# Kernel tuning notes

Measured on AMD Instinct MI355X. Metric: run time of the kernel, lower is better.

Reference implementation:

```python
import jax, jax.numpy as jnp
import numpy as np

K_HEADS = 8
D_HEAD = 64
D = K_HEADS * D_HEAD  # 512
B, TP, TQ, N = 8, 48, 48, 256


def setup_inputs() -> dict:
    key = jax.random.key(0)
    ks = jax.random.split(key, 13)
    s = 1.0 / np.sqrt(D)
    inp = {
        "X": jax.random.normal(ks[0], (B, TP, N, D), jnp.float32),
        "STE_P": jax.random.normal(ks[1], (B, TP, N, D), jnp.float32),
        "STE_Q": jax.random.normal(ks[2], (B, TQ, N, D), jnp.float32),
        "Wq": jax.random.uniform(ks[3], (D, D), jnp.float32, -s, s),
        "bq": jax.random.uniform(ks[4], (D,), jnp.float32, -s, s),
        "Wk": jax.random.uniform(ks[5], (D, D), jnp.float32, -s, s),
        "bk": jax.random.uniform(ks[6], (D,), jnp.float32, -s, s),
        "Wv": jax.random.uniform(ks[7], (D, D), jnp.float32, -s, s),
        "bv": jax.random.uniform(ks[8], (D,), jnp.float32, -s, s),
        "W1": jax.random.uniform(ks[9], (D, D), jnp.float32, -s, s),
        "b1": jax.random.uniform(ks[10], (D,), jnp.float32, -s, s),
        "W2": jax.random.uniform(ks[11], (D, D), jnp.float32, -s, s),
        "b2": jax.random.uniform(ks[12], (D,), jnp.float32, -s, s),
    }
    return inp


def reference(X, STE_P, STE_Q, Wq, bq, Wk, bk, Wv, bv, W1, b1, W2, b2):
    # ReLU-fused QKV projections
    q = jax.nn.relu(STE_Q @ Wq + bq)  # [B, Tq, N, D]
    k = jax.nn.relu(STE_P @ Wk + bk)  # [B, Tp, N, D]
    v = jax.nn.relu(X @ Wv + bv)      # [B, Tp, N, D]

    # split(last, d) + cat(dim 0) == introduce head axis h of size K
    b, tq, n, _ = q.shape
    tp = k.shape[1]
    q = q.reshape(b, tq, n, K_HEADS, D_HEAD)
    k = k.reshape(b, tp, n, K_HEADS, D_HEAD)
    v = v.reshape(b, tp, n, K_HEADS, D_HEAD)

    # attention over the TIME axis, per node and head: scores [b,h,n,tq,tp]
    scale = 1.0 / jnp.sqrt(jnp.asarray(D_HEAD, q.dtype))
    attn = jnp.einsum('bqnhd,bpnhd->bhnqp', q, k) * scale
    attn = jax.nn.softmax(attn, axis=-1)
    out = jnp.einsum('bhnqp,bpnhd->bqnhd', attn, v).reshape(b, tq, n, D)

    out = jax.nn.relu(out @ W1 + b1) @ W2 + b2
    return out
```

## Files before the change

kernel.cpp:

```cpp
#include <hip/hip_runtime.h>

typedef _Float16 f16;
typedef __fp16 hf2 __attribute__((ext_vector_type(2)));
typedef _Float16 f16x4 __attribute__((ext_vector_type(4)));
typedef _Float16 f16x8 __attribute__((ext_vector_type(8)));
typedef float f32x4 __attribute__((ext_vector_type(4)));

typedef const __attribute__((address_space(1))) unsigned int guint;
typedef __attribute__((address_space(3))) unsigned int luint;
__device__ __forceinline__ void gl_lds16(const void* g, void* l) {
    __builtin_amdgcn_global_load_lds((guint*)g, (luint*)l, 16, 0, 0);
}
template <int N>
__device__ __forceinline__ void vmwait() {
    if constexpr (N == 8)       asm volatile("s_waitcnt vmcnt(8)" ::: "memory");
    else if constexpr (N == 6)  asm volatile("s_waitcnt vmcnt(6)" ::: "memory");
    else if constexpr (N == 4)  asm volatile("s_waitcnt vmcnt(4)" ::: "memory");
    else                        asm volatile("s_waitcnt vmcnt(0)" ::: "memory");
}
__device__ __forceinline__ void barrier_raw() { __builtin_amdgcn_s_barrier(); __builtin_amdgcn_sched_barrier(0); }

__global__ __launch_bounds__(256) void wconv(const float* w0, const float* w1, const float* w2,
                                             const float* w3, const float* w4, f16* dst) {
    const float* src;
    switch (blockIdx.z) { case 0: src = w0; break; case 1: src = w1; break;
                          case 2: src = w2; break; case 3: src = w3; break; default: src = w4; }
    __shared__ float tile[32][33];
    int k0 = blockIdx.x * 32, n0 = blockIdx.y * 32;
    int t = threadIdx.x;
    int r = t >> 3, c4 = (t & 7) * 4;
    float4 v = *(const float4*)(src + (k0 + r) * 512 + n0 + c4);
    tile[r][c4 + 0] = v.x; tile[r][c4 + 1] = v.y; tile[r][c4 + 2] = v.z; tile[r][c4 + 3] = v.w;
    __syncthreads();
    f16x4 o;
    o[0] = (f16)tile[c4 + 0][r]; o[1] = (f16)tile[c4 + 1][r];
    o[2] = (f16)tile[c4 + 2][r]; o[3] = (f16)tile[c4 + 3][r];
    *(f16x4*)(dst + (size_t)blockIdx.z * 262144 + (n0 + r) * 512 + k0 + c4) = o;
}

__global__ __launch_bounds__(512, 1) void gemm_qkv(const float* __restrict__ A,
                                                   const f16* __restrict__ Bt,
                                                   const float* __restrict__ bias,
                                                   f16* __restrict__ Cp) {
    constexpr int ASZ = 32768;
    constexpr int BUFSZ = ASZ + 16384;
    __shared__ __align__(16) char smem[3 * BUFSZ];

    const int cpx = gridDim.x >> 3;
    const int orig = blockIdx.x;
    const int wgid = (orig & 7) * cpx + (orig >> 3);
    const int by = wgid & 1;
    const int bx = wgid >> 1;
    const int r0 = bx * 256, c0 = by * 256;

    const int t = threadIdx.x;
    const int j = t & 63, w = t >> 6;
    const int lr = j & 15, lq = j >> 4;
    const int wr = (w >> 2) * 128, wc = (w & 3) * 64;

    const float* aS = A + (size_t)(r0 + (t >> 3)) * 512 + ((t & 7) ^ ((t >> 3) & 7)) * 4;
    const f16* bS = Bt + (size_t)(c0 + (t >> 2)) * 512 + ((t & 3) ^ ((t >> 3) & 3)) * 8;
    const int dstT = t * 16;

    int aoffL[8], aoffH[8], boff[4];
#pragma unroll
    for (int m = 0; m < 8; m++) {
        int row = wr + m * 16 + lr;
        int s = row & 7;
        aoffL[m] = row * 128 + (((2 * lq) ^ s) << 4);
        aoffH[m] = row * 128 + (((2 * lq + 1) ^ s) << 4);
    }
#pragma unroll
    for (int nb = 0; nb < 4; nb++) {
        int row = wc + nb * 16 + lr;
        boff[nb] = ASZ + row * 64 + ((lq ^ ((row >> 1) & 3)) << 4);
    }

    f32x4 acc[8][4] = {};

    auto stageA = [&](int kt, int buf) {
        char* d = smem + buf * BUFSZ + dstT;
        const float* s = aS + kt * 32;
#pragma unroll
        for (int i = 0; i < 4; i++) gl_lds16(s + (size_t)i * 64 * 512, d + i * 8192);
    };
    auto stageB = [&](int kt, int buf) {
        char* d = smem + buf * BUFSZ + ASZ + dstT;
        const f16* s = bS + kt * 32;
        gl_lds16(s, d);
        gl_lds16(s + 65536, d + 8192);
    };

    auto loadA4 = [&](const char* sb, int m0, f16x8* afr) {
#pragma unroll
        for (int m = 0; m < 4; m++) {
            float4 x0 = *(const float4*)(sb + aoffL[m0 + m]);
            float4 x1 = *(const float4*)(sb + aoffH[m0 + m]);
            hf2 p0 = __builtin_amdgcn_cvt_pkrtz(x0.x, x0.y);
            hf2 p1 = __builtin_amdgcn_cvt_pkrtz(x0.z, x0.w);
            hf2 p2 = __builtin_amdgcn_cvt_pkrtz(x1.x, x1.y);
            hf2 p3 = __builtin_amdgcn_cvt_pkrtz(x1.z, x1.w);
            f16x8 h;
            h[0] = (f16)p0[0]; h[1] = (f16)p0[1]; h[2] = (f16)p1[0]; h[3] = (f16)p1[1];
            h[4] = (f16)p2[0]; h[5] = (f16)p2[1]; h[6] = (f16)p3[0]; h[7] = (f16)p3[1];
            afr[m] = h;
        }
    };

    stageA(0, 0); stageB(0, 0); stageA(1, 1); stageB(1, 1);

    int bufc = 0;
#pragma unroll 1
    for (int kt = 0; kt < 16; ++kt) {
        const char* sb = smem + bufc * BUFSZ;
        const int bufs = (bufc == 2) ? 0 : bufc + 1;
        const int bufs2 = (bufs == 2) ? 0 : bufs + 1;
        if (kt < 15) vmwait<6>(); else vmwait<0>();
        barrier_raw();
        if (kt < 14) stageA(kt + 2, bufs2);
        f16x8 bfr[4], afr[4];
#pragma unroll
        for (int nb = 0; nb < 4; nb++) bfr[nb] = *(const f16x8*)(sb + boff[nb]);
        loadA4(sb, 0, afr);
        __builtin_amdgcn_s_setprio(1);
#pragma unroll
        for (int m = 0; m < 4; m++)
#pragma unroll
            for (int nb = 0; nb < 4; nb++)
                acc[m][nb] = __builtin_amdgcn_mfma_f32_16x16x32_f16(afr[m], bfr[nb], acc[m][nb], 0, 0, 0);
        __builtin_amdgcn_s_setprio(0);
        barrier_raw();
        if (kt < 14) stageB(kt + 2, bufs2);
        f16x8 afr2[4];
        loadA4(sb, 4, afr2);
        __builtin_amdgcn_s_setprio(1);
#pragma unroll
        for (int m = 0; m < 4; m++)
#pragma unroll
            for (int nb = 0; nb < 4; nb++)
                acc[m + 4][nb] = __builtin_amdgcn_mfma_f32_16x16x32_f16(afr2[m], bfr[nb], acc[m + 4][nb], 0, 0, 0);
        __builtin_amdgcn_s_setprio(0);
        bufc = bufs;
    }

#pragma unroll
    for (int nb = 0; nb < 4; nb++) {
        int col = c0 + wc + nb * 16 + lr;
        float b = bias[col];
#pragma unroll
        for (int m = 0; m < 8; m++) {
#pragma unroll
            for (int r = 0; r < 4; r++) {
                float v = fmaxf(acc[m][nb][r] + b, 0.0f);
                size_t row = (size_t)(r0 + wr + m * 16 + lq * 4 + r);
                Cp[row * 512 + col] = (f16)v;
            }
        }
    }
}

template <bool RELU, bool O16>
__global__ __launch_bounds__(512, 2) void gemm_8ph(const f16* __restrict__ A,
                                                   const f16* __restrict__ Bt,
                                                   const float* __restrict__ bias,
                                                   void* __restrict__ Cp) {
    constexpr int BUFSZ = 32768;
    __shared__ __align__(16) char smem[4 * BUFSZ];

    const int cpx = gridDim.x >> 3;
    const int orig = blockIdx.x;
    const int wgid = (orig & 7) * cpx + (orig >> 3);
    const int by = wgid & 1;
    const int bx = wgid >> 1;
    const int r0 = bx * 256, c0 = by * 256;

    const int t = threadIdx.x;
    const int j = t & 63, w = t >> 6;
    const int lr = j & 15, lq = j >> 4;
    const int wr = (w >> 2) * 128, wc = (w & 3) * 64;

    const int srow = t >> 2;
    const int sblk = (t & 3) ^ ((t >> 3) & 3);
    const f16* aS = A  + (size_t)(r0 + srow) * 512 + sblk * 8;
    const f16* bS = Bt + (size_t)(c0 + srow) * 512 + sblk * 8;
    const int dstT = t * 16;

    int aoff[8], boff[4];
#pragma unroll
    for (int m = 0; m < 8; m++) {
        int row = wr + m * 16 + lr;
        aoff[m] = row * 64 + ((lq ^ ((row >> 1) & 3)) << 4);
    }
#pragma unroll
    for (int nb = 0; nb < 4; nb++) {
        int row = wc + nb * 16 + lr;
        boff[nb] = 16384 + row * 64 + ((lq ^ ((row >> 1) & 3)) << 4);
    }

    f32x4 acc[8][4] = {};

    auto stageA = [&](int kt) {
        char* d = smem + (kt & 3) * BUFSZ + dstT;
        const f16* s = aS + kt * 32;
        gl_lds16(s, d);
        gl_lds16(s + 65536, d + 8192);
    };
    auto stageB = [&](int kt) {
        char* d = smem + (kt & 3) * BUFSZ + 16384 + dstT;
        const f16* s = bS + kt * 32;
        gl_lds16(s, d);
        gl_lds16(s + 65536, d + 8192);
    };

    stageA(0); stageB(0); stageA(1); stageB(1); stageA(2); stageB(2);

#pragma unroll 1
    for (int kt = 0; kt < 16; ++kt) {
        const char* sb = smem + (kt & 3) * BUFSZ;
        if (kt <= 13)      vmwait<8>();
        else if (kt == 14) vmwait<4>();
        else               vmwait<0>();
        barrier_raw();
        if (kt < 13) stageA(kt + 3);
        f16x8 bfr[4], afr[4];
#pragma unroll
        for (int nb = 0; nb < 4; nb++) bfr[nb] = *(const f16x8*)(sb + boff[nb]);
#pragma unroll
        for (int m = 0; m < 4; m++) afr[m] = *(const f16x8*)(sb + aoff[m]);
        __builtin_amdgcn_s_setprio(1);
#pragma unroll
        for (int m = 0; m < 4; m++)
#pragma unroll
            for (int nb = 0; nb < 4; nb++)
                acc[m][nb] = __builtin_amdgcn_mfma_f32_16x16x32_f16(afr[m], bfr[nb], acc[m][nb], 0, 0, 0);
        __builtin_amdgcn_s_setprio(0);
        barrier_raw();
        if (kt < 13) stageB(kt + 3);
        f16x8 afr2[4];
#pragma unroll
        for (int m = 0; m < 4; m++) afr2[m] = *(const f16x8*)(sb + aoff[m + 4]);
        __builtin_amdgcn_s_setprio(1);
#pragma unroll
        for (int m = 0; m < 4; m++)
#pragma unroll
            for (int nb = 0; nb < 4; nb++)
                acc[m + 4][nb] = __builtin_amdgcn_mfma_f32_16x16x32_f16(afr2[m], bfr[nb], acc[m + 4][nb], 0, 0, 0);
        __builtin_amdgcn_s_setprio(0);
    }

#pragma unroll
    for (int nb = 0; nb < 4; nb++) {
        int col = c0 + wc + nb * 16 + lr;
        float b = bias[col];
#pragma unroll
        for (int m = 0; m < 8; m++) {
#pragma unroll
            for (int r = 0; r < 4; r++) {
                float v = acc[m][nb][r] + b;
                if (RELU) v = fmaxf(v, 0.0f);
                size_t row = (size_t)(r0 + wr + m * 16 + lq * 4 + r);
                if (O16) ((f16*)Cp)[row * 512 + col] = (f16)v;
                else     ((float*)Cp)[row * 512 + col] = v;
            }
        }
    }
}

__global__ __launch_bounds__(64) void attn_kernel(const f16* __restrict__ q,
                                                  const f16* __restrict__ k,
                                                  const f16* __restrict__ v,
                                                  f16* __restrict__ out) {
    const int h = blockIdx.x, n = blockIdx.y, b = blockIdx.z;
    __shared__ f16 sQ[48 * 72];
    __shared__ f16 sK[48 * 72];
    __shared__ f16 sP[48 * 72];
    __shared__ f16 sVt[64 * 72];
    const int l = threadIdx.x, lr = l & 15, lq = l >> 4;
    const size_t rowstride = 256 * 512;
    const size_t base = ((size_t)(b * 48) * 256 + n) * 512 + h * 64;

    const int pr = l >> 3, pc = (l & 7) * 8;
#pragma unroll
    for (int pass = 0; pass < 6; pass++) {
        int row = pass * 8 + pr;
        size_t g = base + (size_t)row * rowstride + pc;
        f16x8 qv = *(const f16x8*)(q + g);
        f16x8 kv = *(const f16x8*)(k + g);
        f16x8 vv = *(const f16x8*)(v + g);
        *(f16x8*)&sQ[row * 72 + pc] = qv;
        *(f16x8*)&sK[row * 72 + pc] = kv;
#pragma unroll
        for (int jj = 0; jj < 8; jj++) sVt[(pc + jj) * 72 + row] = vv[jj];
    }
    {
        f16x8 z = {};
        *(f16x8*)&sVt[l * 72 + 48] = z;
        *(f16x8*)&sVt[l * 72 + 56] = z;
        if (l < 48) { *(f16x8*)&sP[l * 72 + 48] = z; *(f16x8*)&sP[l * 72 + 56] = z; }
    }
    __syncthreads();

    f32x4 s[3][3] = {};
#pragma unroll
    for (int ks = 0; ks < 2; ks++) {
        f16x8 aq[3], bk[3];
#pragma unroll
        for (int m = 0; m < 3; m++)  aq[m] = *(const f16x8*)&sQ[(m * 16 + lr) * 72 + ks * 32 + lq * 8];
#pragma unroll
        for (int nb = 0; nb < 3; nb++) bk[nb] = *(const f16x8*)&sK[(nb * 16 + lr) * 72 + ks * 32 + lq * 8];
#pragma unroll
        for (int m = 0; m < 3; m++)
#pragma unroll
            for (int nb = 0; nb < 3; nb++)
                s[m][nb] = __builtin_amdgcn_mfma_f32_16x16x32_f16(aq[m], bk[nb], s[m][nb], 0, 0, 0);
    }

#pragma unroll
    for (int m = 0; m < 3; m++) {
#pragma unroll
        for (int r = 0; r < 4; r++) {
            float a0 = s[m][0][r] * 0.125f, a1 = s[m][1][r] * 0.125f, a2 = s[m][2][r] * 0.125f;
            float mx = fmaxf(a0, fmaxf(a1, a2));
#pragma unroll
            for (int d = 1; d < 16; d <<= 1) mx = fmaxf(mx, __shfl_xor(mx, d));
            float e0 = __expf(a0 - mx), e1 = __expf(a1 - mx), e2 = __expf(a2 - mx);
            float sm = e0 + e1 + e2;
#pragma unroll
            for (int d = 1; d < 16; d <<= 1) sm += __shfl_xor(sm, d);
            float inv = 1.0f / sm;
            int row = m * 16 + lq * 4 + r;
            sP[row * 72 + 0  + lr] = (f16)(e0 * inv);
            sP[row * 72 + 16 + lr] = (f16)(e1 * inv);
            sP[row * 72 + 32 + lr] = (f16)(e2 * inv);
        }
    }
    __syncthreads();

    f32x4 o[3][4] = {};
#pragma unroll
    for (int ks = 0; ks < 2; ks++) {
        f16x8 ap[3], bvv[4];
#pragma unroll
        for (int m = 0; m < 3; m++)  ap[m] = *(const f16x8*)&sP[(m * 16 + lr) * 72 + ks * 32 + lq * 8];
#pragma unroll
        for (int nb = 0; nb < 4; nb++) bvv[nb] = *(const f16x8*)&sVt[(nb * 16 + lr) * 72 + ks * 32 + lq * 8];
#pragma unroll
        for (int m = 0; m < 3; m++)
#pragma unroll
            for (int nb = 0; nb < 4; nb++)
                o[m][nb] = __builtin_amdgcn_mfma_f32_16x16x32_f16(ap[m], bvv[nb], o[m][nb], 0, 0, 0);
    }

#pragma unroll
    for (int m = 0; m < 3; m++)
#pragma unroll
        for (int nb = 0; nb < 4; nb++)
#pragma unroll
            for (int r = 0; r < 4; r++) {
                int row = m * 16 + lq * 4 + r;
                out[base + (size_t)row * rowstride + nb * 16 + lr] = (f16)o[m][nb][r];
            }
}

extern "C" void kernel_launch(void* const* d_in, const int* in_sizes, int n_in,
                              void* d_out, int out_size, void* d_ws, size_t ws_size,
                              hipStream_t stream) {
    const float* X    = (const float*)d_in[0];
    const float* STEP = (const float*)d_in[1];
    const float* STEQ = (const float*)d_in[2];
    const float* Wq   = (const float*)d_in[3];
    const float* bq   = (const float*)d_in[4];
    const float* Wk   = (const float*)d_in[5];
    const float* bk   = (const float*)d_in[6];
    const float* Wv   = (const float*)d_in[7];
    const float* bv   = (const float*)d_in[8];
    const float* W1   = (const float*)d_in[9];
    const float* b1   = (const float*)d_in[10];
    const float* W2   = (const float*)d_in[11];
    const float* b2   = (const float*)d_in[12];
    float* out = (float*)d_out;

    const size_t MROWS = 98304;
    f16* ws  = (f16*)d_ws;
    f16* Wqt = ws;
    f16* Wkt = ws + 262144;
    f16* Wvt = ws + 524288;
    f16* W1t = ws + 786432;
    f16* W2t = ws + 1048576;
    f16* qb  = ws + 1310720;
    f16* kb  = qb + MROWS * 512;
    f16* vb  = kb + MROWS * 512;
    f16* attn = qb;
    f16* hb   = kb;

    wconv<<<dim3(16, 16, 5), 256, 0, stream>>>(Wq, Wk, Wv, W1, W2, ws);

    gemm_qkv<<<768, 512, 0, stream>>>(STEQ, Wqt, bq, qb);
    gemm_qkv<<<768, 512, 0, stream>>>(STEP, Wkt, bk, kb);
    gemm_qkv<<<768, 512, 0, stream>>>(X,    Wvt, bv, vb);

    attn_kernel<<<dim3(8, 256, 8), 64, 0, stream>>>(qb, kb, vb, attn);

    gemm_8ph<true,  true ><<<768, 512, 0, stream>>>(attn, W1t, b1, hb);
    gemm_8ph<false, false><<<768, 512, 0, stream>>>(hb,   W2t, b2, out);
}
```

Measured before the change: 674.6 us.

## Pre-convert QKV inputs to fp16 and use full-width 128-row GEMM tiles

A new conv3 kernel converts STE_Q, STE_P and X from fp32 to fp16 into the q/k/v workspace buffers. The QKV projection GEMM is replaced by gemm_f512, which reads fp16 A and computes a 128x512 output tile per block, writing in place over its own input rows. This removes the per-tile fp32-to-fp16 conversion and the large fp32 A staging in LDS. Because each block now covers all 512 output columns, A is read once per GEMM instead of once per column half. The cost is an extra pass over the activations to write and re-read fp16 copies, plus one more kernel launch.

```diff
diff --git a/kernel.cpp b/kernel.cpp
--- a/kernel.cpp
+++ b/kernel.cpp
@@ -14,11 +14,22 @@
 template <int N>
 __device__ __forceinline__ void vmwait() {
     if constexpr (N == 8)       asm volatile("s_waitcnt vmcnt(8)" ::: "memory");
-    else if constexpr (N == 6)  asm volatile("s_waitcnt vmcnt(6)" ::: "memory");
+    else if constexpr (N == 5)  asm volatile("s_waitcnt vmcnt(5)" ::: "memory");
     else if constexpr (N == 4)  asm volatile("s_waitcnt vmcnt(4)" ::: "memory");
     else                        asm volatile("s_waitcnt vmcnt(0)" ::: "memory");
 }
 __device__ __forceinline__ void barrier_raw() { __builtin_amdgcn_s_barrier(); __builtin_amdgcn_sched_barrier(0); }
+
+__device__ __forceinline__ f16x8 pack8(float4 x0, float4 x1) {
+    hf2 p0 = __builtin_amdgcn_cvt_pkrtz(x0.x, x0.y);
+    hf2 p1 = __builtin_amdgcn_cvt_pkrtz(x0.z, x0.w);
+    hf2 p2 = __builtin_amdgcn_cvt_pkrtz(x1.x, x1.y);
+    hf2 p3 = __builtin_amdgcn_cvt_pkrtz(x1.z, x1.w);
+    f16x8 h;
+    h[0] = (f16)p0[0]; h[1] = (f16)p0[1]; h[2] = (f16)p1[0]; h[3] = (f16)p1[1];
+    h[4] = (f16)p2[0]; h[5] = (f16)p2[1]; h[6] = (f16)p3[0]; h[7] = (f16)p3[1];
+    return h;
+}
 
 __global__ __launch_bounds__(256) void wconv(const float* w0, const float* w1, const float* w2,
                                              const float* w3, const float* w4, f16* dst) {
@@ -38,117 +49,122 @@
     *(f16x4*)(dst + (size_t)blockIdx.z * 262144 + (n0 + r) * 512 + k0 + c4) = o;
 }
 
-__global__ __launch_bounds__(512, 1) void gemm_qkv(const float* __restrict__ A,
-                                                   const f16* __restrict__ Bt,
-                                                   const float* __restrict__ bias,
-                                                   f16* __restrict__ Cp) {
-    constexpr int ASZ = 32768;
-    constexpr int BUFSZ = ASZ + 16384;
+__global__ __launch_bounds__(256) void conv3(const float* __restrict__ a0, const float* __restrict__ a1,
+                                             const float* __restrict__ a2, f16* __restrict__ d0,
+                                             f16* __restrict__ d1, f16* __restrict__ d2) {
+    const float* s; f16* d;
+    if (blockIdx.y == 0)      { s = a0; d = d0; }
+    else if (blockIdx.y == 1) { s = a1; d = d1; }
+    else                      { s = a2; d = d2; }
+    const int n8 = 6291456;
+    int i = blockIdx.x * 256 + threadIdx.x;
+    const int stride = gridDim.x * 256;
+    for (; i < n8; i += stride) {
+        const float4* p = (const float4*)(s + (size_t)i * 8);
+        float4 x0 = p[0], x1 = p[1];
+        *(f16x8*)(d + (size_t)i * 8) = pack8(x0, x1);
+    }
+}
+
+__global__ __launch_bounds__(512, 1) void gemm_f512(const f16* __restrict__ A,
+                                                    const f16* __restrict__ Bt,
+                                                    const float* __restrict__ bias,
+                                                    f16* __restrict__ Cp) {
+    constexpr int ASZ = 8192;
+    constexpr int BSZ = 32768;
+    constexpr int BUFSZ = ASZ + BSZ;
     __shared__ __align__(16) char smem[3 * BUFSZ];
 
     const int cpx = gridDim.x >> 3;
     const int orig = blockIdx.x;
-    const int wgid = (orig & 7) * cpx + (orig >> 3);
-    const int by = wgid & 1;
-    const int bx = wgid >> 1;
-    const int r0 = bx * 256, c0 = by * 256;
+    const int bx = (orig & 7) * cpx + (orig >> 3);
+    const int r0 = bx * 128;
 
     const int t = threadIdx.x;
     const int j = t & 63, w = t >> 6;
     const int lr = j & 15, lq = j >> 4;
-    const int wr = (w >> 2) * 128, wc = (w & 3) * 64;
-
-    const float* aS = A + (size_t)(r0 + (t >> 3)) * 512 + ((t & 7) ^ ((t >> 3) & 7)) * 4;
-    const f16* bS = Bt + (size_t)(c0 + (t >> 2)) * 512 + ((t & 3) ^ ((t >> 3) & 3)) * 8;
+    const int wr = (w >> 2) * 64, wc = (w & 3) * 128;
+
+    const int sblk = (t & 3) ^ ((t >> 3) & 3);
+    const f16* aS = A  + (size_t)(r0 + (t >> 2)) * 512 + sblk * 8;
+    const f16* bS = Bt + (size_t)(t >> 2) * 512 + sblk * 8;
     const int dstT = t * 16;
 
-    int aoffL[8], aoffH[8], boff[4];
-#pragma unroll
-    for (int m = 0; m < 8; m++) {
+    int aoff[4], boff[8];
+#pragma unroll
+    for (int m = 0; m < 4; m++) {
         int row = wr + m * 16 + lr;
-        int s = row & 7;
-        aoffL[m] = row * 128 + (((2 * lq) ^ s) << 4);
-        aoffH[m] = row * 128 + (((2 * lq + 1) ^ s) << 4);
-    }
-#pragma unroll
-    for (int nb = 0; nb < 4; nb++) {
+        aoff[m] = row * 64 + ((lq ^ ((row >> 1) & 3)) << 4);
+    }
+#pragma unroll
+    for (int nb = 0; nb < 8; nb++) {
         int row = wc + nb * 16 + lr;
         boff[nb] = ASZ + row * 64 + ((lq ^ ((row >> 1) & 3)) << 4);
     }
 
-    f32x4 acc[8][4] = {};
+    f32x4 acc[4][8] = {};
 
     auto stageA = [&](int kt, int buf) {
-        char* d = smem + buf * BUFSZ + dstT;
-        const float* s = aS + kt * 32;
-#pragma unroll
-        for (int i = 0; i < 4; i++) gl_lds16(s + (size_t)i * 64 * 512, d + i * 8192);
+        gl_lds16(aS + kt * 32, smem + buf * BUFSZ + dstT);
     };
-    auto stageB = [&](int kt, int buf) {
+    auto stageB01 = [&](int kt, int buf) {
         char* d = smem + buf * BUFSZ + ASZ + dstT;
         const f16* s = bS + kt * 32;
         gl_lds16(s, d);
         gl_lds16(s + 65536, d + 8192);
     };
-
-    auto loadA4 = [&](const char* sb, int m0, f16x8* afr) {
-#pragma unroll
-        for (int m = 0; m < 4; m++) {
-            float4 x0 = *(const float4*)(sb + aoffL[m0 + m]);
-            float4 x1 = *(const float4*)(sb + aoffH[m0 + m]);
-            hf2 p0 = __builtin_amdgcn_cvt_pkrtz(x0.x, x0.y);
-            hf2 p1 = __builtin_amdgcn_cvt_pkrtz(x0.z, x0.w);
-            hf2 p2 = __builtin_amdgcn_cvt_pkrtz(x1.x, x1.y);
-            hf2 p3 = __builtin_amdgcn_cvt_pkrtz(x1.z, x1.w);
-            f16x8 h;
-            h[0] = (f16)p0[0]; h[1] = (f16)p0[1]; h[2] = (f16)p1[0]; h[3] = (f16)p1[1];
-            h[4] = (f16)p2[0]; h[5] = (f16)p2[1]; h[6] = (f16)p3[0]; h[7] = (f16)p3[1];
-            afr[m] = h;
-        }
+    auto stageB23 = [&](int kt, int buf) {
+        char* d = smem + buf * BUFSZ + ASZ + dstT;
+        const f16* s = bS + kt * 32;
+        gl_lds16(s + 131072, d + 16384);
+        gl_lds16(s + 196608, d + 24576);
     };
 
-    stageA(0, 0); stageB(0, 0); stageA(1, 1); stageB(1, 1);
+    stageA(0, 0); stageB01(0, 0); stageB23(0, 0);
+    stageA(1, 1); stageB01(1, 1); stageB23(1, 1);
 
     int bufc = 0;
 #pragma unroll 1
     for (int kt = 0; kt < 16; ++kt) {
         const char* sb = smem + bufc * BUFSZ;
-        const int bufs = (bufc == 2) ? 0 : bufc + 1;
-        const int bufs2 = (bufs == 2) ? 0 : bufs + 1;
-        if (kt < 15) vmwait<6>(); else vmwait<0>();
+        const int b1 = (bufc == 2) ? 0 : bufc + 1;
+        const int bufs2 = (b1 == 2) ? 0 : b1 + 1;
+        if (kt < 15) vmwait<5>(); else vmwait<0>();
         barrier_raw();
-        if (kt < 14) stageA(kt + 2, bufs2);
-        f16x8 bfr[4], afr[4];
-#pragma unroll
-        for (int nb = 0; nb < 4; nb++) bfr[nb] = *(const f16x8*)(sb + boff[nb]);
-        loadA4(sb, 0, afr);
+        if (kt < 14) { stageA(kt + 2, bufs2); stageB01(kt + 2, bufs2); }
+        f16x8 bfr[8], afr[2];
+#pragma unroll
+        for (int nb = 0; nb < 8; nb++) bfr[nb] = *(const f16x8*)(sb + boff[nb]);
+#pragma unroll
+        for (int m = 0; m < 2; m++) afr[m] = *(const f16x8*)(sb + aoff[m]);
         __builtin_amdgcn_s_setprio(1);
 #pragma unroll
-        for (int m = 0; m < 4; m++)
-#pragma unroll
-            for (int nb = 0; nb < 4; nb++)
+        for (int m = 0; m < 2; m++)
+#pragma unroll
+            for (int nb = 0; nb < 8; nb++)
                 acc[m][nb] = __builtin_amdgcn_mfma_f32_16x16x32_f16(afr[m], bfr[nb], acc[m][nb], 0, 0, 0);
         __builtin_amdgcn_s_setprio(0);
         barrier_raw();
-        if (kt < 14) stageB(kt + 2, bufs2);
-        f16x8 afr2[4];
-        loadA4(sb, 4, afr2);
+        if (kt < 14) stageB23(kt + 2, bufs2);
+        f16x8 afr2[2];
+#pragma unroll
+        for (int m = 0; m < 2; m++) afr2[m] = *(const f16x8*)(sb + aoff[m + 2]);
         __builtin_amdgcn_s_setprio(1);
 #pragma unroll
-        for (int m = 0; m < 4; m++)
-#pragma unroll
-            for (int nb = 0; nb < 4; nb++)
-                acc[m + 4][nb] = __builtin_amdgcn_mfma_f32_16x16x32_f16(afr2[m], bfr[nb], acc[m + 4][nb], 0, 0, 0);
+        for (int m = 0; m < 2; m++)
+#pragma unroll
+            for (int nb = 0; nb < 8; nb++)
+                acc[m + 2][nb] = __builtin_amdgcn_mfma_f32_16x16x32_f16(afr2[m], bfr[nb], acc[m + 2][nb], 0, 0, 0);
         __builtin_amdgcn_s_setprio(0);
-        bufc = bufs;
-    }
-
-#pragma unroll
-    for (int nb = 0; nb < 4; nb++) {
-        int col = c0 + wc + nb * 16 + lr;
+        bufc = b1;
+    }
+
+#pragma unroll
+    for (int nb = 0; nb < 8; nb++) {
+        int col = wc + nb * 16 + lr;
         float b = bias[col];
 #pragma unroll
-        for (int m = 0; m < 8; m++) {
+        for (int m = 0; m < 4; m++) {
 #pragma unroll
             for (int r = 0; r < 4; r++) {
                 float v = fmaxf(acc[m][nb][r] + b, 0.0f);
@@ -390,17 +406,18 @@
     f16* qb  = ws + 1310720;
     f16* kb  = qb + MROWS * 512;
     f16* vb  = kb + MROWS * 512;
-    f16* attn = qb;
-    f16* hb   = kb;
+    f16* hb  = kb;
 
     wconv<<<dim3(16, 16, 5), 256, 0, stream>>>(Wq, Wk, Wv, W1, W2, ws);
 
-    gemm_qkv<<<768, 512, 0, stream>>>(STEQ, Wqt, bq, qb);
-    gemm_qkv<<<768, 512, 0, stream>>>(STEP, Wkt, bk, kb);
-    gemm_qkv<<<768, 512, 0, stream>>>(X,    Wvt, bv, vb);
-
-    attn_kernel<<<dim3(8, 256, 8), 64, 0, stream>>>(qb, kb, vb, attn);
-
-    gemm_8ph<true,  true ><<<768, 512, 0, stream>>>(attn, W1t, b1, hb);
-    gemm_8ph<false, false><<<768, 512, 0, stream>>>(hb,   W2t, b2, out);
-}
+    conv3<<<dim3(2048, 3), 256, 0, stream>>>(STEQ, STEP, X, qb, kb, vb);
+
+    gemm_f512<<<768, 512, 0, stream>>>(qb, Wqt, bq, qb);
+    gemm_f512<<<768, 512, 0, stream>>>(kb, Wkt, bk, kb);
+    gemm_f512<<<768, 512, 0, stream>>>(vb, Wvt, bv, vb);
+
+    attn_kernel<<<dim3(8, 256, 8), 64, 0, stream>>>(qb, kb, vb, qb);
+
+    gemm_8ph<true,  true ><<<768, 512, 0, stream>>>(qb, W1t, b1, hb);
+    gemm_8ph<false, false><<<768, 512, 0, stream>>>(hb, W2t, b2, out);
+}
```

After: 696.6 us. 1.03x slower.

## Load fp32 A operand directly into registers in smaller-tile QKV GEMM

Applied to the files above, without the earlier changes.

Replaces the 256x256-tile QKV projection GEMM, which staged fp32 A tiles through LDS, with a 128x128-tile, 256-thread kernel. Each wave now loads its A rows from global memory straight into registers (double-buffered) and packs them to fp16, while only the fp16 B tile goes through a 4-deep LDS ring via global_load_lds. This removes the LDS traffic and footprint for the large fp32 operand and raises occupancy through smaller blocks and more of them. In exchange, per-lane global loads are less coalesced and B is reused across a smaller tile.

```diff
diff --git a/kernel.cpp b/kernel.cpp
--- a/kernel.cpp
+++ b/kernel.cpp
@@ -13,12 +13,23 @@
 }
 template <int N>
 __device__ __forceinline__ void vmwait() {
-    if constexpr (N == 8)       asm volatile("s_waitcnt vmcnt(8)" ::: "memory");
-    else if constexpr (N == 6)  asm volatile("s_waitcnt vmcnt(6)" ::: "memory");
+    if constexpr (N == 12)      asm volatile("s_waitcnt vmcnt(12)" ::: "memory");
+    else if constexpr (N == 8)  asm volatile("s_waitcnt vmcnt(8)" ::: "memory");
     else if constexpr (N == 4)  asm volatile("s_waitcnt vmcnt(4)" ::: "memory");
     else                        asm volatile("s_waitcnt vmcnt(0)" ::: "memory");
 }
 __device__ __forceinline__ void barrier_raw() { __builtin_amdgcn_s_barrier(); __builtin_amdgcn_sched_barrier(0); }
+
+__device__ __forceinline__ f16x8 pack8(float4 x0, float4 x1) {
+    hf2 p0 = __builtin_amdgcn_cvt_pkrtz(x0.x, x0.y);
+    hf2 p1 = __builtin_amdgcn_cvt_pkrtz(x0.z, x0.w);
+    hf2 p2 = __builtin_amdgcn_cvt_pkrtz(x1.x, x1.y);
+    hf2 p3 = __builtin_amdgcn_cvt_pkrtz(x1.z, x1.w);
+    f16x8 h;
+    h[0] = (f16)p0[0]; h[1] = (f16)p0[1]; h[2] = (f16)p1[0]; h[3] = (f16)p1[1];
+    h[4] = (f16)p2[0]; h[5] = (f16)p2[1]; h[6] = (f16)p3[0]; h[7] = (f16)p3[1];
+    return h;
+}
 
 __global__ __launch_bounds__(256) void wconv(const float* w0, const float* w1, const float* w2,
                                              const float* w3, const float* w4, f16* dst) {
@@ -38,109 +49,83 @@
     *(f16x4*)(dst + (size_t)blockIdx.z * 262144 + (n0 + r) * 512 + k0 + c4) = o;
 }
 
-__global__ __launch_bounds__(512, 1) void gemm_qkv(const float* __restrict__ A,
-                                                   const f16* __restrict__ Bt,
-                                                   const float* __restrict__ bias,
-                                                   f16* __restrict__ Cp) {
-    constexpr int ASZ = 32768;
-    constexpr int BUFSZ = ASZ + 16384;
-    __shared__ __align__(16) char smem[3 * BUFSZ];
+__global__ __launch_bounds__(256) void gemm_areg(const float* __restrict__ A,
+                                                 const f16* __restrict__ Bt,
+                                                 const float* __restrict__ bias,
+                                                 f16* __restrict__ Cp) {
+    __shared__ __align__(16) char smem[4 * 8192];
 
     const int cpx = gridDim.x >> 3;
     const int orig = blockIdx.x;
     const int wgid = (orig & 7) * cpx + (orig >> 3);
-    const int by = wgid & 1;
-    const int bx = wgid >> 1;
-    const int r0 = bx * 256, c0 = by * 256;
-
-    const int t = threadIdx.x;
-    const int j = t & 63, w = t >> 6;
+    const int by = wgid & 3, bx = wgid >> 2;
+    const int r0 = bx * 128, c0 = by * 128;
+
+    const int t = threadIdx.x, j = t & 63, w = t >> 6;
     const int lr = j & 15, lq = j >> 4;
-    const int wr = (w >> 2) * 128, wc = (w & 3) * 64;
-
-    const float* aS = A + (size_t)(r0 + (t >> 3)) * 512 + ((t & 7) ^ ((t >> 3) & 7)) * 4;
+    const int wr = (w >> 1) * 64, wc = (w & 1) * 64;
+
     const f16* bS = Bt + (size_t)(c0 + (t >> 2)) * 512 + ((t & 3) ^ ((t >> 3) & 3)) * 8;
-    const int dstT = t * 16;
-
-    int aoffL[8], aoffH[8], boff[4];
-#pragma unroll
-    for (int m = 0; m < 8; m++) {
-        int row = wr + m * 16 + lr;
-        int s = row & 7;
-        aoffL[m] = row * 128 + (((2 * lq) ^ s) << 4);
-        aoffH[m] = row * 128 + (((2 * lq + 1) ^ s) << 4);
-    }
+    const float* aBase = A + (size_t)(r0 + wr + lr) * 512 + lq * 8;
+
+    int boff[4];
 #pragma unroll
     for (int nb = 0; nb < 4; nb++) {
         int row = wc + nb * 16 + lr;
-        boff[nb] = ASZ + row * 64 + ((lq ^ ((row >> 1) & 3)) << 4);
-    }
-
-    f32x4 acc[8][4] = {};
-
-    auto stageA = [&](int kt, int buf) {
-        char* d = smem + buf * BUFSZ + dstT;
-        const float* s = aS + kt * 32;
-#pragma unroll
-        for (int i = 0; i < 4; i++) gl_lds16(s + (size_t)i * 64 * 512, d + i * 8192);
-    };
-    auto stageB = [&](int kt, int buf) {
-        char* d = smem + buf * BUFSZ + ASZ + dstT;
-        const f16* s = bS + kt * 32;
-        gl_lds16(s, d);
-        gl_lds16(s + 65536, d + 8192);
-    };
-
-    auto loadA4 = [&](const char* sb, int m0, f16x8* afr) {
+        boff[nb] = row * 64 + ((lq ^ ((row >> 1) & 3)) << 4);
+    }
+
+    f32x4 acc[4][4] = {};
+    float4 a0[4][2], a1[4][2];
+
+    auto stageB = [&](int s) {
+        char* d = smem + (s & 3) * 8192 + t * 16;
+        const f16* src = bS + s * 32;
+        gl_lds16(src, d);
+        gl_lds16(src + 32768, d + 4096);
+    };
+    auto loadA = [&](int s, float4 (*ar)[2]) {
 #pragma unroll
         for (int m = 0; m < 4; m++) {
-            float4 x0 = *(const float4*)(sb + aoffL[m0 + m]);
-            float4 x1 = *(const float4*)(sb + aoffH[m0 + m]);
-            hf2 p0 = __builtin_amdgcn_cvt_pkrtz(x0.x, x0.y);
-            hf2 p1 = __builtin_amdgcn_cvt_pkrtz(x0.z, x0.w);
-            hf2 p2 = __builtin_amdgcn_cvt_pkrtz(x1.x, x1.y);
-            hf2 p3 = __builtin_amdgcn_cvt_pkrtz(x1.z, x1.w);
-            f16x8 h;
-            h[0] = (f16)p0[0]; h[1] = (f16)p0[1]; h[2] = (f16)p1[0]; h[3] = (f16)p1[1];
-            h[4] = (f16)p2[0]; h[5] = (f16)p2[1]; h[6] = (f16)p3[0]; h[7] = (f16)p3[1];
-            afr[m] = h;
+            const float* p = aBase + (size_t)m * 16 * 512 + s * 32;
+            ar[m][0] = *(const float4*)p;
+            ar[m][1] = *(const float4*)(p + 4);
         }
     };
-
-    stageA(0, 0); stageB(0, 0); stageA(1, 1); stageB(1, 1);
-
-    int bufc = 0;
+    auto compute = [&](int s, float4 (*ar)[2]) {
+        const char* sb = smem + (s & 3) * 8192;
+        f16x8 bv[4], av[4];
+#pragma unroll
+        for (int nb = 0; nb < 4; nb++) bv[nb] = *(const f16x8*)(sb + boff[nb]);
+#pragma unroll
+        for (int m = 0; m < 4; m++) av[m] = pack8(ar[m][0], ar[m][1]);
+        __builtin_amdgcn_s_setprio(1);
+#pragma unroll
+        for (int m = 0; m < 4; m++)
+#pragma unroll
+            for (int nb = 0; nb < 4; nb++)
+                acc[m][nb] = __builtin_amdgcn_mfma_f32_16x16x32_f16(av[m], bv[nb], acc[m][nb], 0, 0, 0);
+        __builtin_amdgcn_s_setprio(0);
+    };
+
+    loadA(0, a0);
+    stageB(0); stageB(1); stageB(2);
+
 #pragma unroll 1
-    for (int kt = 0; kt < 16; ++kt) {
-        const char* sb = smem + bufc * BUFSZ;
-        const int bufs = (bufc == 2) ? 0 : bufc + 1;
-        const int bufs2 = (bufs == 2) ? 0 : bufs + 1;
-        if (kt < 15) vmwait<6>(); else vmwait<0>();
+    for (int kt = 0; kt < 16; kt += 2) {
+        if (kt < 15) loadA(kt + 1, a1);
         barrier_raw();
-        if (kt < 14) stageA(kt + 2, bufs2);
-        f16x8 bfr[4], afr[4];
-#pragma unroll
-        for (int nb = 0; nb < 4; nb++) bfr[nb] = *(const f16x8*)(sb + boff[nb]);
-        loadA4(sb, 0, afr);
-        __builtin_amdgcn_s_setprio(1);
-#pragma unroll
-        for (int m = 0; m < 4; m++)
-#pragma unroll
-            for (int nb = 0; nb < 4; nb++)
-                acc[m][nb] = __builtin_amdgcn_mfma_f32_16x16x32_f16(afr[m], bfr[nb], acc[m][nb], 0, 0, 0);
-        __builtin_amdgcn_s_setprio(0);
+        stageB(kt + 3 <= 15 ? kt + 3 : 15);
+        if (kt < 14) vmwait<12>(); else vmwait<0>();
+        __builtin_amdgcn_sched_barrier(0);
+        compute(kt, a0);
+        if (kt + 2 < 16) loadA(kt + 2, a0);
         barrier_raw();
-        if (kt < 14) stageB(kt + 2, bufs2);
-        f16x8 afr2[4];
-        loadA4(sb, 4, afr2);
-        __builtin_amdgcn_s_setprio(1);
-#pragma unroll
-        for (int m = 0; m < 4; m++)
-#pragma unroll
-            for (int nb = 0; nb < 4; nb++)
-                acc[m + 4][nb] = __builtin_amdgcn_mfma_f32_16x16x32_f16(afr2[m], bfr[nb], acc[m + 4][nb], 0, 0, 0);
-        __builtin_amdgcn_s_setprio(0);
-        bufc = bufs;
+        if (kt + 4 <= 15) stageB(kt + 4);
+        else if (kt + 1 < 15) stageB(15);
+        if (kt < 14) vmwait<12>(); else vmwait<0>();
+        __builtin_amdgcn_sched_barrier(0);
+        compute(kt + 1, a1);
     }
 
 #pragma unroll
@@ -148,7 +133,7 @@
         int col = c0 + wc + nb * 16 + lr;
         float b = bias[col];
 #pragma unroll
-        for (int m = 0; m < 8; m++) {
+        for (int m = 0; m < 4; m++) {
 #pragma unroll
             for (int r = 0; r < 4; r++) {
                 float v = fmaxf(acc[m][nb][r] + b, 0.0f);
@@ -381,6 +366,7 @@
     float* out = (float*)d_out;
 
     const size_t MROWS = 98304;
+    const size_t MBUF  = MROWS * 512;
     f16* ws  = (f16*)d_ws;
     f16* Wqt = ws;
     f16* Wkt = ws + 262144;
@@ -388,19 +374,18 @@
     f16* W1t = ws + 786432;
     f16* W2t = ws + 1048576;
     f16* qb  = ws + 1310720;
-    f16* kb  = qb + MROWS * 512;
-    f16* vb  = kb + MROWS * 512;
-    f16* attn = qb;
-    f16* hb   = kb;
+    f16* kb  = qb + MBUF;
+    f16* vb  = kb + MBUF;
+    f16* hb  = kb;
 
     wconv<<<dim3(16, 16, 5), 256, 0, stream>>>(Wq, Wk, Wv, W1, W2, ws);
 
-    gemm_qkv<<<768, 512, 0, stream>>>(STEQ, Wqt, bq, qb);
-    gemm_qkv<<<768, 512, 0, stream>>>(STEP, Wkt, bk, kb);
-    gemm_qkv<<<768, 512, 0, stream>>>(X,    Wvt, bv, vb);
-
-    attn_kernel<<<dim3(8, 256, 8), 64, 0, stream>>>(qb, kb, vb, attn);
-
-    gemm_8ph<true,  true ><<<768, 512, 0, stream>>>(attn, W1t, b1, hb);
-    gemm_8ph<false, false><<<768, 512, 0, stream>>>(hb,   W2t, b2, out);
-}
+    gemm_areg<<<3072, 256, 0, stream>>>(STEQ, Wqt, bq, qb);
+    gemm_areg<<<3072, 256, 0, stream>>>(STEP, Wkt, bk, kb);
+    gemm_areg<<<3072, 256, 0, stream>>>(X,    Wvt, bv, vb);
+
+    attn_kernel<<<dim3(8, 256, 8), 64, 0, stream>>>(qb, kb, vb, qb);
+
+    gemm_8ph<true,  true ><<<768, 512, 0, stream>>>(qb, W1t, b1, hb);
+    gemm_8ph<false, false><<<768, 512, 0, stream>>>(hb, W2t, b2, out);
+}
```

Result: slower. 941.0 us (+39.5%).
